# Kernel optimization log

Hardware: AMD Instinct MI355X
Metric: run time of the kernel (lower is better)

## Reference

```python
import jax, jax.numpy as jnp
import numpy as np

NUM_USERS = 100000
NUM_ITEMS = 50000
EMB_DIM = 64
NUM_LAYERS = 3
NUM_EDGES = 1000000


def _xavier(key, shape):
    fan_in, fan_out = shape[-1], shape[-2] if len(shape) > 1 else shape[-1]
    limit = float(np.sqrt(6.0 / (fan_in + fan_out)))
    return jax.random.uniform(key, shape, jnp.float32, -limit, limit)


def setup_inputs() -> dict:
    key = jax.random.key(0)
    ks = jax.random.split(key, 8)
    edge_u = jax.random.randint(ks[0], (NUM_EDGES,), 0, NUM_USERS)
    edge_i = jax.random.randint(ks[1], (NUM_EDGES,), 0, NUM_ITEMS)
    u_emb = _xavier(ks[2], (NUM_USERS, EMB_DIM))
    i_emb = _xavier(ks[3], (NUM_ITEMS, EMB_DIM))
    Wgc = _xavier(ks[4], (NUM_LAYERS, EMB_DIM, EMB_DIM))
    Wbi = _xavier(ks[5], (NUM_LAYERS, EMB_DIM, EMB_DIM))
    bgc = jnp.zeros((NUM_LAYERS, EMB_DIM), jnp.float32)
    bbi = jnp.zeros((NUM_LAYERS, EMB_DIM), jnp.float32)
    return {"u_emb": u_emb, "i_emb": i_emb, "Wgc": Wgc, "bgc": bgc,
            "Wbi": Wbi, "bbi": bbi, "edge_u": edge_u, "edge_i": edge_i}


def _smooth(X, src, dst, dv_isqrt, de_inv, num_v, num_e):
    # HGNN smoothing: D_v^{-1/2} H D_e^{-1} H^T D_v^{-1/2} X via edge list
    X1 = X * dv_isqrt[:, None]
    E = jax.ops.segment_sum(X1[src], dst, num_segments=num_e) * de_inv[:, None]
    Y = jax.ops.segment_sum(E[dst], src, num_segments=num_v)
    return Y * dv_isqrt[:, None]


def reference(u_emb, i_emb, Wgc, bgc, Wbi, bbi, edge_u, edge_i):
    NU, NI, D = u_emb.shape[0], i_emb.shape[0], u_emb.shape[1]
    ones = jnp.ones((edge_u.shape[0],), jnp.float32)
    deg_u = jax.ops.segment_sum(ones, edge_u, num_segments=NU)
    deg_i = jax.ops.segment_sum(ones, edge_i, num_segments=NI)
    du_isqrt = jnp.where(deg_u > 0, deg_u, 1.0) ** -0.5 * (deg_u > 0)
    di_isqrt = jnp.where(deg_i > 0, deg_i, 1.0) ** -0.5 * (deg_i > 0)
    du_inv = jnp.where(deg_u > 0, 1.0 / jnp.where(deg_u > 0, deg_u, 1.0), 0.0)
    di_inv = jnp.where(deg_i > 0, 1.0 / jnp.where(deg_i > 0, deg_i, 1.0), 0.0)

    all_embs = jnp.concatenate([u_emb, i_emb], axis=0)
    embs_list = [all_embs]
    for l in range(Wgc.shape[0]):
        u, i = all_embs[:NU], all_embs[NU:]
        # hg_ui: users = vertices, items = hyperedges
        u_s = _smooth(u, edge_u, edge_i, du_isqrt, di_inv, NU, NI)
        # hg_iu: items = vertices, users = hyperedges
        i_s = _smooth(i, edge_i, edge_u, di_isqrt, du_inv, NI, NU)
        g = jnp.concatenate([u_s, i_s], axis=0)
        sum_embs = jax.nn.leaky_relu(g @ Wgc[l].T + bgc[l] + all_embs, negative_slope=0.2)
        bi_embs = jax.nn.leaky_relu((all_embs * g) @ Wbi[l].T + bbi[l], negative_slope=0.2)
        all_embs = sum_embs + bi_embs  # dropout off (eval mode)
        norm = jnp.sqrt(jnp.sum(all_embs * all_embs, axis=1, keepdims=True))
        all_embs = all_embs / jnp.maximum(norm, 1e-12)
        embs_list.append(all_embs)
    embs = jnp.mean(jnp.stack(embs_list, axis=1), axis=1)
    return embs[:NU], embs[NU:]
```

## Files before the change

### kernel.cpp

```cpp
#include <hip/hip_runtime.h>
#include <cstdint>
#include <cstddef>

#define NU 100000
#define NI 50000
#define NTOT 150000
#define EDIM 64
#define NE 1000000
#define NLAYERS 3
#define NTILES (NTOT / 16)
#define NPAIR (NTOT / 2)

#define NBKT 256
#define NPB 586
#define NSHARD 1
#define BCAP 13312
#define BCUR_STRIDE 16
#define BIN_EPB 1024
#define BIN_NBLK ((NE + BIN_EPB - 1) / BIN_EPB)
#define LCAP 28
#define LPAD 29
#define SLICE_CAP 13312

typedef __attribute__((ext_vector_type(8))) short short8;
typedef __attribute__((ext_vector_type(4))) float floatx4;

__device__ inline unsigned short f2bf(float f) {
    unsigned u = __float_as_uint(f);
    u += 0x7fffu + ((u >> 16) & 1u);
    return (unsigned short)(u >> 16);
}
__device__ inline unsigned pack_bf2(float a, float b) {
    unsigned ua = __float_as_uint(a); ua += 0x7fffu + ((ua >> 16) & 1u);
    unsigned ub = __float_as_uint(b); ub += 0x7fffu + ((ub >> 16) & 1u);
    return (ua >> 16) | (ub & 0xffff0000u);
}
__device__ inline float bf_lo(unsigned u) { return __uint_as_float(u << 16); }
__device__ inline float bf_hi(unsigned u) { return __uint_as_float(u & 0xffff0000u); }

__global__ __launch_bounds__(256) void k_binpairs(const int* __restrict__ eu,
                                                  const int* __restrict__ ei,
                                                  unsigned* __restrict__ bcur,
                                                  unsigned* __restrict__ bbuf) {
    __shared__ unsigned lbuf[NBKT * LPAD];
    __shared__ int lcnt[NBKT];
    int t = threadIdx.x;
    if (t < NBKT) lcnt[t] = 0;
    __syncthreads();
    int ebase = blockIdx.x * BIN_EPB + t;
#pragma unroll
    for (int k = 0; k < 4; ++k) {
        int e = ebase + k * 256;
        if (e < NE) {
            int u = eu[e];
            int v = NU + ei[e];
            int b0 = u / NPB;
            int w0 = ((u - b0 * NPB) << 18) | v;
            int p0 = atomicAdd(&lcnt[b0], 1);
            if (p0 < LCAP) lbuf[b0 * LPAD + p0] = (unsigned)w0;
            else {
                unsigned gp = atomicAdd(&bcur[b0 * BCUR_STRIDE], 1u);
                if (gp < BCAP) bbuf[(size_t)b0 * BCAP + gp] = (unsigned)w0;
            }
            int b1 = v / NPB;
            int w1 = ((v - b1 * NPB) << 18) | u;
            int p1 = atomicAdd(&lcnt[b1], 1);
            if (p1 < LCAP) lbuf[b1 * LPAD + p1] = (unsigned)w1;
            else {
                unsigned gp = atomicAdd(&bcur[b1 * BCUR_STRIDE], 1u);
                if (gp < BCAP) bbuf[(size_t)b1 * BCAP + gp] = (unsigned)w1;
            }
        }
    }
    __syncthreads();
    int nb = min(lcnt[t], LCAP);
    if (nb > 0) {
        unsigned gp = atomicAdd(&bcur[t * BCUR_STRIDE], (unsigned)nb);
        for (int i = 0; i < nb; ++i) {
            unsigned idx = gp + i;
            if (idx < BCAP) bbuf[(size_t)t * BCAP + idx] = lbuf[t * LPAD + i];
        }
    }
}

__global__ void k_bktprefix(const unsigned* __restrict__ bcur, int* __restrict__ bktbase) {
    __shared__ int sm[256];
    int t = threadIdx.x;
    int tot = (int)bcur[t * BCUR_STRIDE];
    if (tot > BCAP) tot = BCAP;
    sm[t] = tot;
    __syncthreads();
    for (int off = 1; off < 256; off <<= 1) {
        int tmp = (t >= off) ? sm[t - off] : 0;
        __syncthreads();
        sm[t] += tmp;
        __syncthreads();
    }
    bktbase[t] = sm[t] - tot;
}

__global__ __launch_bounds__(1024) void k_buildcsr(
    const unsigned* __restrict__ bbuf, const unsigned* __restrict__ bcur,
    const int* __restrict__ bktbase, int* __restrict__ deg, int* __restrict__ start,
    float* __restrict__ isq, float* __restrict__ inv, int* __restrict__ csr) {
    __shared__ int slice[SLICE_CAP];
    __shared__ int lcur[NPB];
    __shared__ int scnt_s;
    int b = blockIdx.x;
    int t = threadIdx.x;
    int n0 = b * NPB;
    int nn = NTOT - n0;
    if (nn > NPB) nn = NPB;
    if (nn < 0) nn = 0;
    if (t < NPB) lcur[t] = 0;
    if (t == 0) {
        int c = (int)bcur[b * BCUR_STRIDE];
        scnt_s = c < BCAP ? c : BCAP;
    }
    __syncthreads();
    int c = scnt_s;
    const unsigned* pb = bbuf + (size_t)b * BCAP;
    for (int i = t; i < c; i += 1024) atomicAdd(&lcur[(int)(pb[i] >> 18)], 1);
    __syncthreads();
    int cnt_t = (t < nn) ? lcur[t] : 0;
    slice[t] = cnt_t;
    __syncthreads();
    for (int off = 1; off < 1024; off <<= 1) {
        int tmp = (t >= off) ? slice[t - off] : 0;
        __syncthreads();
        slice[t] += tmp;
        __syncthreads();
    }
    int excl = slice[t] - cnt_t;
    int slen = slice[1023];
    int bb = bktbase[b];
    if (t < nn) {
        int n = n0 + t;
        deg[n] = cnt_t;
        start[n] = bb + excl;
        float df = (float)cnt_t;
        isq[n] = cnt_t > 0 ? 1.0f / sqrtf(df) : 0.f;
        inv[n] = cnt_t > 0 ? 1.0f / df : 0.f;
    }
    __syncthreads();
    if (t < nn) lcur[t] = excl;
    __syncthreads();
    for (int i = t; i < c; i += 1024) {
        unsigned pr = pb[i];
        int idx = atomicAdd(&lcur[(int)(pr >> 18)], 1);
        if (idx < SLICE_CAP) slice[idx] = (int)(pr & 0x3FFFFu);
    }
    __syncthreads();
    if (slen > SLICE_CAP) slen = SLICE_CAP;
    for (int i = t; i < slen; i += 1024) csr[bb + i] = slice[i];
}

__global__ void k_init(const float* __restrict__ ue, const float* __restrict__ ie,
                       const float* __restrict__ isq,
                       unsigned* __restrict__ snap0, unsigned* gbuf,
                       const float* __restrict__ Wg, const float* __restrict__ Wb,
                       unsigned short* __restrict__ wgb, unsigned short* __restrict__ wbb,
                       unsigned* __restrict__ Ebuf) {
    int i = blockIdx.x * blockDim.x + threadIdx.x;
    const int n4 = NTOT * EDIM / 4;
    const int nw4 = NLAYERS * 4096 / 4;
    if (i < nw4) {
        float4 g4 = ((const float4*)Wg)[i];
        float4 b4 = ((const float4*)Wb)[i];
        uint2 g, b;
        g.x = pack_bf2(g4.x, g4.y); g.y = pack_bf2(g4.z, g4.w);
        b.x = pack_bf2(b4.x, b4.y); b.y = pack_bf2(b4.z, b4.w);
        ((uint2*)wgb)[i] = g;
        ((uint2*)wbb)[i] = b;
    }
    if (i < 16) {
        ((uint2*)(Ebuf + NTOT * 32))[i] = make_uint2(0u, 0u);
        ((uint2*)(gbuf + NTOT * 32))[i] = make_uint2(0u, 0u);
    }
    if (i < n4) {
        const int nu4 = NU * EDIM / 4;
        float4 v = (i < nu4) ? ((const float4*)ue)[i] : ((const float4*)ie)[i - nu4];
        float s = isq[i >> 4];
        uint2 b, bs;
        b.x = pack_bf2(v.x, v.y);
        b.y = pack_bf2(v.z, v.w);
        bs.x = pack_bf2(v.x * s, v.y * s);
        bs.y = pack_bf2(v.z * s, v.w * s);
        ((uint2*)snap0)[i] = b;
        ((uint2*)gbuf)[i] = bs;
    }
}

__global__ __launch_bounds__(256) void k_gather(
    const unsigned* __restrict__ in_bf, unsigned* __restrict__ out_bf,
    const int* __restrict__ csr, const int* __restrict__ start,
    const int* __restrict__ deg, const float* __restrict__ sA) {
    int gw = (blockIdx.x * 256 + threadIdx.x) >> 6;
    int lane = threadIdx.x & 63;
    if (gw >= NPAIR) return;
    int l2 = lane & 31;
    int hbase = lane & 32;
    int row = gw * 2 + (lane >> 5);
    int s0 = start[row];
    int dg = deg[row];
    int dgo = __shfl_xor(dg, 32);
    int dgmax = max(dg, dgo);
    float acc0 = 0.f, acc1 = 0.f;
    for (int j0 = 0; j0 < dgmax; j0 += 32) {
        int nidx = NTOT;
        if (j0 + l2 < dg) nidx = csr[s0 + j0 + l2];
        int jlim = min(32, dgmax - j0);
        for (int j = 0; j < jlim; j += 16) {
            int mm[16];
            unsigned uu[16];
#pragma unroll
            for (int k = 0; k < 16; ++k)
                mm[k] = __shfl(nidx, hbase + j + k);
#pragma unroll
            for (int k = 0; k < 16; ++k)
                uu[k] = in_bf[mm[k] * 32 + l2];
#pragma unroll
            for (int k = 0; k < 16; ++k) {
                acc0 += bf_lo(uu[k]);
                acc1 += bf_hi(uu[k]);
            }
        }
    }
    float s = sA[row];
    out_bf[row * 32 + l2] = pack_bf2(s * acc0, s * acc1);
}

__global__ __launch_bounds__(256) void k_dense_mfma(
    const unsigned short* __restrict__ a_prev, unsigned* gbuf,
    unsigned short* __restrict__ snap_l, const float* __restrict__ isq,
    const unsigned short* __restrict__ wgb, const unsigned short* __restrict__ wbb,
    const float* __restrict__ bg, const float* __restrict__ bb, int writeScaled,
    int finalOut, const unsigned short* __restrict__ s1,
    const float* __restrict__ ue, const float* __restrict__ ie,
    float* __restrict__ outp) {
    int lane = threadIdx.x & 63;
    int lanelo = lane & 15;
    int quad = lane >> 4;
    int wid = (blockIdx.x * blockDim.x + threadIdx.x) >> 6;
    if (wid >= NTILES) return;

    short8 bWg[4][2], bWb[4][2];
#pragma unroll
    for (int t = 0; t < 4; ++t) {
#pragma unroll
        for (int h = 0; h < 2; ++h) {
            int n = t * 16 + lanelo;
            int k0 = h * 32 + quad * 8;
            bWg[t][h] = *(const short8*)&wgb[n * 64 + k0];
            bWb[t][h] = *(const short8*)&wbb[n * 64 + k0];
        }
    }
    float bgv[4], bbv[4];
#pragma unroll
    for (int t = 0; t < 4; ++t) {
        bgv[t] = bg[t * 16 + lanelo];
        bbv[t] = bb[t * 16 + lanelo];
    }

    int rbase = wid * 16;
    int arow = rbase + lanelo;
    short8 aG[2], aAG[2];
#pragma unroll
    for (int h = 0; h < 2; ++h) {
        uint4 ug = *(const uint4*)(gbuf + arow * 32 + h * 16 + quad * 4);
        uint4 ua = *(const uint4*)((const unsigned*)a_prev + arow * 32 + h * 16 + quad * 4);
        aG[h] = *(const short8*)&ug;
        uint4 up;
        up.x = pack_bf2(bf_lo(ua.x) * bf_lo(ug.x), bf_hi(ua.x) * bf_hi(ug.x));
        up.y = pack_bf2(bf_lo(ua.y) * bf_lo(ug.y), bf_hi(ua.y) * bf_hi(ug.y));
        up.z = pack_bf2(bf_lo(ua.z) * bf_lo(ug.z), bf_hi(ua.z) * bf_hi(ug.z));
        up.w = pack_bf2(bf_lo(ua.w) * bf_lo(ug.w), bf_hi(ua.w) * bf_hi(ug.w));
        aAG[h] = *(const short8*)&up;
    }
    floatx4 accg[4], accb[4];
#pragma unroll
    for (int t = 0; t < 4; ++t) {
        accg[t] = (floatx4)(0.f);
        accb[t] = (floatx4)(0.f);
    }
#pragma unroll
    for (int t = 0; t < 4; ++t) {
#pragma unroll
        for (int h = 0; h < 2; ++h) {
            accg[t] = __builtin_amdgcn_mfma_f32_16x16x32_bf16(aG[h], bWg[t][h], accg[t], 0, 0, 0);
            accb[t] = __builtin_amdgcn_mfma_f32_16x16x32_bf16(aAG[h], bWb[t][h], accb[t], 0, 0, 0);
        }
    }
    float nv[4][4];
    float ss[4] = {0.f, 0.f, 0.f, 0.f};
#pragma unroll
    for (int i = 0; i < 4; ++i) {
        int r = rbase + quad * 4 + i;
#pragma unroll
        for (int t = 0; t < 4; ++t) {
            float a = __uint_as_float((unsigned)a_prev[r * 64 + t * 16 + lanelo] << 16);
            float e1 = accg[t][i] + bgv[t] + a;
            e1 = e1 >= 0.f ? e1 : 0.2f * e1;
            float e2 = accb[t][i] + bbv[t];
            e2 = e2 >= 0.f ? e2 : 0.2f * e2;
            float v = e1 + e2;
            nv[i][t] = v;
            ss[i] += v * v;
        }
    }
#pragma unroll
    for (int m = 1; m < 16; m <<= 1) {
#pragma unroll
        for (int i = 0; i < 4; ++i) ss[i] += __shfl_xor(ss[i], m, 64);
    }
#pragma unroll
    for (int i = 0; i < 4; ++i) {
        int r = rbase + quad * 4 + i;
        float rn = 1.0f / fmaxf(sqrtf(ss[i]), 1e-12f);
        float sc = isq[r] * rn;
        if (finalOut) {
#pragma unroll
            for (int t = 0; t < 4; ++t) {
                int idx = r * 64 + t * 16 + lanelo;
                float rr = nv[i][t] * rn;
                float s1v = __uint_as_float((unsigned)s1[idx] << 16);
                float s2v = __uint_as_float((unsigned)a_prev[idx] << 16);
                float ev = (r < NU) ? ue[idx] : ie[idx - NU * 64];
                outp[idx] = 0.25f * (ev + s1v + s2v + rr);
            }
        } else {
#pragma unroll
            for (int t = 0; t < 4; ++t) {
                int idx = r * 64 + t * 16 + lanelo;
                float rr = nv[i][t] * rn;
                snap_l[idx] = f2bf(rr);
                if (writeScaled)
                    ((unsigned short*)gbuf)[idx] = f2bf(nv[i][t] * sc);
            }
        }
    }
}


extern "C" void kernel_launch(void* const* d_in, const int* in_sizes, int n_in,
                              void* d_out, int out_size, void* d_ws, size_t ws_size,
                              hipStream_t stream) {
    const float* u_emb = (const float*)d_in[0];
    const float* i_emb = (const float*)d_in[1];
    const float* Wgc = (const float*)d_in[2];
    const float* bgc = (const float*)d_in[3];
    const float* Wbi = (const float*)d_in[4];
    const float* bbi = (const float*)d_in[5];
    const int* edge_u = (const int*)d_in[6];
    const int* edge_i = (const int*)d_in[7];
    float* out = (float*)d_out;

    char* w = (char*)d_ws;
    auto alloc = [&](size_t bytes) {
        char* p = w;
        w += (bytes + 255) & ~(size_t)255;
        return p;
    };
    const size_t ROWBYTES = (size_t)(NTOT + 1) * EDIM * 2;
    int* deg = (int*)alloc((size_t)NTOT * 4);
    int* start = (int*)alloc((size_t)NTOT * 4);
    unsigned* bcur = (unsigned*)alloc((size_t)NBKT * BCUR_STRIDE * 4);
    int* bktbase = (int*)alloc(256 * 4);
    int* csr = (int*)alloc((size_t)2 * NE * 4);
    float* isq = (float*)alloc((size_t)NTOT * 4);
    float* inv = (float*)alloc((size_t)NTOT * 4);
    unsigned short* wgb = (unsigned short*)alloc((size_t)NLAYERS * 4096 * 2);
    unsigned short* wbb = (unsigned short*)alloc((size_t)NLAYERS * 4096 * 2);
    unsigned* snap0 = (unsigned*)alloc((size_t)NTOT * EDIM * 2);
    unsigned* snap1 = (unsigned*)alloc((size_t)NTOT * EDIM * 2);
    unsigned* snap2 = (unsigned*)alloc((size_t)NTOT * EDIM * 2);
    unsigned* Ebuf = (unsigned*)alloc(ROWBYTES);
    unsigned* gbuf = (unsigned*)alloc(ROWBYTES);
    unsigned* bbuf = (unsigned*)snap1;

    hipMemsetAsync(bcur, 0, (size_t)NBKT * BCUR_STRIDE * 4, stream);
    k_binpairs<<<BIN_NBLK, 256, 0, stream>>>(edge_u, edge_i, bcur, bbuf);
    k_bktprefix<<<1, 256, 0, stream>>>(bcur, bktbase);
    k_buildcsr<<<NBKT, 1024, 0, stream>>>(bbuf, bcur, bktbase, deg, start, isq, inv, csr);
    k_init<<<(NTOT * EDIM / 4 + 255) / 256, 256, 0, stream>>>(
        u_emb, i_emb, isq, snap0, gbuf, Wgc, Wbi, wgb, wbb, Ebuf);

    const int gatherBlocks = (NPAIR * 64 + 255) / 256;
    const int denseBlocks = (NTILES * 64 + 255) / 256;
    const unsigned short* aprev[3] = {(unsigned short*)snap0, (unsigned short*)snap1,
                                      (unsigned short*)snap2};
    unsigned short* snaps[3] = {(unsigned short*)snap1, (unsigned short*)snap2,
                                (unsigned short*)snap1 };
    for (int l = 0; l < NLAYERS; ++l) {
        k_gather<<<gatherBlocks, 256, 0, stream>>>(gbuf, Ebuf, csr, start, deg, inv);
        k_gather<<<gatherBlocks, 256, 0, stream>>>(Ebuf, gbuf, csr, start, deg, isq);
        k_dense_mfma<<<denseBlocks, 256, 0, stream>>>(
            aprev[l], gbuf, snaps[l], isq, wgb + (size_t)l * 4096, wbb + (size_t)l * 4096,
            bgc + (size_t)l * 64, bbi + (size_t)l * 64,
            l < NLAYERS - 1 ? 1 : 0,
            l == NLAYERS - 1 ? 1 : 0,
            (const unsigned short*)snap1, u_emb, i_emb, out);
    }
}
```

Baseline: 468.4 us.

## Fuse second gather into dense MFMA kernel and fold prefix/init into CSR build

Removes the second per-layer gather kernel by having the dense MFMA kernel compute each row's neighbor sum from the CSR directly in its A-fragment layout, so the intermediate gbuf no longer makes a round trip through memory. Also folds the bucket prefix scan and the embedding/weight bf16 init into the CSR build kernel, cutting two launches. In exchange the gather inside the dense kernel uses 16 lanes per row with 4-deep unrolling, so it may expose less memory parallelism and suffer load imbalance from the max degree across 16 rows. Init work is now concentrated in 256 large blocks instead of many small ones.

```diff
diff --git a/kernel.cpp b/kernel.cpp
--- a/kernel.cpp
+++ b/kernel.cpp
@@ -13,7 +13,6 @@
 
 #define NBKT 256
 #define NPB 586
-#define NSHARD 1
 #define BCAP 13312
 #define BCUR_STRIDE 16
 #define BIN_EPB 1024
@@ -83,42 +82,42 @@
     }
 }
 
-__global__ void k_bktprefix(const unsigned* __restrict__ bcur, int* __restrict__ bktbase) {
-    __shared__ int sm[256];
-    int t = threadIdx.x;
-    int tot = (int)bcur[t * BCUR_STRIDE];
-    if (tot > BCAP) tot = BCAP;
-    sm[t] = tot;
-    __syncthreads();
-    for (int off = 1; off < 256; off <<= 1) {
-        int tmp = (t >= off) ? sm[t - off] : 0;
-        __syncthreads();
-        sm[t] += tmp;
-        __syncthreads();
-    }
-    bktbase[t] = sm[t] - tot;
-}
-
 __global__ __launch_bounds__(1024) void k_buildcsr(
     const unsigned* __restrict__ bbuf, const unsigned* __restrict__ bcur,
-    const int* __restrict__ bktbase, int* __restrict__ deg, int* __restrict__ start,
-    float* __restrict__ isq, float* __restrict__ inv, int* __restrict__ csr) {
+    int* __restrict__ deg, int* __restrict__ start,
+    float* __restrict__ isq, float* __restrict__ inv, int* __restrict__ csr,
+    const float* __restrict__ ue, const float* __restrict__ ie,
+    unsigned* __restrict__ snap0, unsigned* __restrict__ gbuf,
+    unsigned* __restrict__ Ebuf,
+    const float* __restrict__ Wg, const float* __restrict__ Wb,
+    unsigned short* __restrict__ wgb, unsigned short* __restrict__ wbb) {
     __shared__ int slice[SLICE_CAP];
     __shared__ int lcur[NPB];
-    __shared__ int scnt_s;
+    __shared__ float sisq[NPB];
+    __shared__ int bb_s, scnt_s;
     int b = blockIdx.x;
     int t = threadIdx.x;
     int n0 = b * NPB;
     int nn = NTOT - n0;
     if (nn > NPB) nn = NPB;
     if (nn < 0) nn = 0;
+    if (t < NBKT) slice[t] = min((int)bcur[t * BCUR_STRIDE], BCAP);
     if (t < NPB) lcur[t] = 0;
+    __syncthreads();
+    for (int off = 1; off < NBKT; off <<= 1) {
+        int tmp = (t < NBKT && t >= off) ? slice[t - off] : 0;
+        __syncthreads();
+        if (t < NBKT) slice[t] += tmp;
+        __syncthreads();
+    }
     if (t == 0) {
-        int c = (int)bcur[b * BCUR_STRIDE];
-        scnt_s = c < BCAP ? c : BCAP;
+        int tb = min((int)bcur[b * BCUR_STRIDE], BCAP);
+        scnt_s = tb;
+        bb_s = slice[b] - tb;
     }
     __syncthreads();
     int c = scnt_s;
+    int bb = bb_s;
     const unsigned* pb = bbuf + (size_t)b * BCAP;
     for (int i = t; i < c; i += 1024) atomicAdd(&lcur[(int)(pb[i] >> 18)], 1);
     __syncthreads();
@@ -133,13 +132,14 @@
     }
     int excl = slice[t] - cnt_t;
     int slen = slice[1023];
-    int bb = bktbase[b];
     if (t < nn) {
         int n = n0 + t;
         deg[n] = cnt_t;
         start[n] = bb + excl;
         float df = (float)cnt_t;
-        isq[n] = cnt_t > 0 ? 1.0f / sqrtf(df) : 0.f;
+        float q = cnt_t > 0 ? 1.0f / sqrtf(df) : 0.f;
+        isq[n] = q;
+        sisq[t] = q;
         inv[n] = cnt_t > 0 ? 1.0f / df : 0.f;
     }
     __syncthreads();
@@ -153,41 +153,34 @@
     __syncthreads();
     if (slen > SLICE_CAP) slen = SLICE_CAP;
     for (int i = t; i < slen; i += 1024) csr[bb + i] = slice[i];
-}
-
-__global__ void k_init(const float* __restrict__ ue, const float* __restrict__ ie,
-                       const float* __restrict__ isq,
-                       unsigned* __restrict__ snap0, unsigned* gbuf,
-                       const float* __restrict__ Wg, const float* __restrict__ Wb,
-                       unsigned short* __restrict__ wgb, unsigned short* __restrict__ wbb,
-                       unsigned* __restrict__ Ebuf) {
-    int i = blockIdx.x * blockDim.x + threadIdx.x;
-    const int n4 = NTOT * EDIM / 4;
-    const int nw4 = NLAYERS * 4096 / 4;
-    if (i < nw4) {
-        float4 g4 = ((const float4*)Wg)[i];
-        float4 b4 = ((const float4*)Wb)[i];
-        uint2 g, b;
-        g.x = pack_bf2(g4.x, g4.y); g.y = pack_bf2(g4.z, g4.w);
-        b.x = pack_bf2(b4.x, b4.y); b.y = pack_bf2(b4.z, b4.w);
-        ((uint2*)wgb)[i] = g;
-        ((uint2*)wbb)[i] = b;
-    }
-    if (i < 16) {
-        ((uint2*)(Ebuf + NTOT * 32))[i] = make_uint2(0u, 0u);
-        ((uint2*)(gbuf + NTOT * 32))[i] = make_uint2(0u, 0u);
-    }
-    if (i < n4) {
-        const int nu4 = NU * EDIM / 4;
-        float4 v = (i < nu4) ? ((const float4*)ue)[i] : ((const float4*)ie)[i - nu4];
-        float s = isq[i >> 4];
-        uint2 b, bs;
-        b.x = pack_bf2(v.x, v.y);
-        b.y = pack_bf2(v.z, v.w);
+    for (int idx = t; idx < nn * 16; idx += 1024) {
+        int r = idx >> 4, cc = idx & 15;
+        int n = n0 + r;
+        float4 v = (n < NU) ? ((const float4*)ue)[(size_t)n * 16 + cc]
+                            : ((const float4*)ie)[(size_t)(n - NU) * 16 + cc];
+        float s = sisq[r];
+        uint2 bq, bs;
+        bq.x = pack_bf2(v.x, v.y);
+        bq.y = pack_bf2(v.z, v.w);
         bs.x = pack_bf2(v.x * s, v.y * s);
         bs.y = pack_bf2(v.z * s, v.w * s);
-        ((uint2*)snap0)[i] = b;
-        ((uint2*)gbuf)[i] = bs;
+        ((uint2*)snap0)[(size_t)n * 16 + cc] = bq;
+        ((uint2*)gbuf)[(size_t)n * 16 + cc] = bs;
+    }
+    if (b == 0) {
+        for (int i = t; i < NLAYERS * 4096 / 4; i += 1024) {
+            float4 g4 = ((const float4*)Wg)[i];
+            float4 b4 = ((const float4*)Wb)[i];
+            uint2 g, bq;
+            g.x = pack_bf2(g4.x, g4.y); g.y = pack_bf2(g4.z, g4.w);
+            bq.x = pack_bf2(b4.x, b4.y); bq.y = pack_bf2(b4.z, b4.w);
+            ((uint2*)wgb)[i] = g;
+            ((uint2*)wbb)[i] = bq;
+        }
+        if (t < 16) {
+            ((uint2*)(Ebuf + NTOT * 32))[t] = make_uint2(0u, 0u);
+            ((uint2*)(gbuf + NTOT * 32))[t] = make_uint2(0u, 0u);
+        }
     }
 }
 
@@ -230,9 +223,12 @@
     out_bf[row * 32 + l2] = pack_bf2(s * acc0, s * acc1);
 }
 
-__global__ __launch_bounds__(256) void k_dense_mfma(
+__global__ __launch_bounds__(256) void k_dense_fused(
+    const unsigned* __restrict__ Ebuf,
     const unsigned short* __restrict__ a_prev, unsigned* gbuf,
     unsigned short* __restrict__ snap_l, const float* __restrict__ isq,
+    const int* __restrict__ csr, const int* __restrict__ start,
+    const int* __restrict__ deg,
     const unsigned short* __restrict__ wgb, const unsigned short* __restrict__ wbb,
     const float* __restrict__ bg, const float* __restrict__ bb, int writeScaled,
     int finalOut, const unsigned short* __restrict__ s1,
@@ -243,6 +239,50 @@
     int quad = lane >> 4;
     int wid = (blockIdx.x * blockDim.x + threadIdx.x) >> 6;
     if (wid >= NTILES) return;
+    int rbase = wid * 16;
+    int arow = rbase + lanelo;
+
+    int s0 = start[arow];
+    int dg = deg[arow];
+    int dmax = dg;
+#pragma unroll
+    for (int m = 1; m < 16; m <<= 1) dmax = max(dmax, __shfl_xor(dmax, m));
+    float accL[2][4], accH[2][4];
+#pragma unroll
+    for (int h = 0; h < 2; ++h)
+#pragma unroll
+        for (int j = 0; j < 4; ++j) { accL[h][j] = 0.f; accH[h][j] = 0.f; }
+    for (int i = 0; i < dmax; i += 4) {
+        int mm[4];
+#pragma unroll
+        for (int k = 0; k < 4; ++k)
+            mm[k] = (i + k < dg) ? csr[s0 + i + k] : NTOT;
+        uint4 ea[4], eb[4];
+#pragma unroll
+        for (int k = 0; k < 4; ++k) {
+            ea[k] = *(const uint4*)(Ebuf + (size_t)mm[k] * 32 + quad * 4);
+            eb[k] = *(const uint4*)(Ebuf + (size_t)mm[k] * 32 + 16 + quad * 4);
+        }
+#pragma unroll
+        for (int k = 0; k < 4; ++k) {
+            const unsigned* pa = (const unsigned*)&ea[k];
+            const unsigned* pcb = (const unsigned*)&eb[k];
+#pragma unroll
+            for (int j = 0; j < 4; ++j) {
+                accL[0][j] += bf_lo(pa[j]);  accH[0][j] += bf_hi(pa[j]);
+                accL[1][j] += bf_lo(pcb[j]); accH[1][j] += bf_hi(pcb[j]);
+            }
+        }
+    }
+    float sc0 = isq[arow];
+    uint4 ugq[2];
+#pragma unroll
+    for (int h = 0; h < 2; ++h) {
+        unsigned* w4 = (unsigned*)&ugq[h];
+#pragma unroll
+        for (int j = 0; j < 4; ++j)
+            w4[j] = pack_bf2(sc0 * accL[h][j], sc0 * accH[h][j]);
+    }
 
     short8 bWg[4][2], bWb[4][2];
 #pragma unroll
@@ -261,13 +301,10 @@
         bgv[t] = bg[t * 16 + lanelo];
         bbv[t] = bb[t * 16 + lanelo];
     }
-
-    int rbase = wid * 16;
-    int arow = rbase + lanelo;
     short8 aG[2], aAG[2];
 #pragma unroll
     for (int h = 0; h < 2; ++h) {
-        uint4 ug = *(const uint4*)(gbuf + arow * 32 + h * 16 + quad * 4);
+        uint4 ug = ugq[h];
         uint4 ua = *(const uint4*)((const unsigned*)a_prev + arow * 32 + h * 16 + quad * 4);
         aG[h] = *(const short8*)&ug;
         uint4 up;
@@ -365,7 +402,6 @@
     int* deg = (int*)alloc((size_t)NTOT * 4);
     int* start = (int*)alloc((size_t)NTOT * 4);
     unsigned* bcur = (unsigned*)alloc((size_t)NBKT * BCUR_STRIDE * 4);
-    int* bktbase = (int*)alloc(256 * 4);
     int* csr = (int*)alloc((size_t)2 * NE * 4);
     float* isq = (float*)alloc((size_t)NTOT * 4);
     float* inv = (float*)alloc((size_t)NTOT * 4);
@@ -380,10 +416,9 @@
 
     hipMemsetAsync(bcur, 0, (size_t)NBKT * BCUR_STRIDE * 4, stream);
     k_binpairs<<<BIN_NBLK, 256, 0, stream>>>(edge_u, edge_i, bcur, bbuf);
-    k_bktprefix<<<1, 256, 0, stream>>>(bcur, bktbase);
-    k_buildcsr<<<NBKT, 1024, 0, stream>>>(bbuf, bcur, bktbase, deg, start, isq, inv, csr);
-    k_init<<<(NTOT * EDIM / 4 + 255) / 256, 256, 0, stream>>>(
-        u_emb, i_emb, isq, snap0, gbuf, Wgc, Wbi, wgb, wbb, Ebuf);
+    k_buildcsr<<<NBKT, 1024, 0, stream>>>(bbuf, bcur, deg, start, isq, inv, csr,
+                                          u_emb, i_emb, snap0, gbuf, Ebuf,
+                                          Wgc, Wbi, wgb, wbb);
 
     const int gatherBlocks = (NPAIR * 64 + 255) / 256;
     const int denseBlocks = (NTILES * 64 + 255) / 256;
@@ -393,9 +428,9 @@
                                 (unsigned short*)snap1 };
     for (int l = 0; l < NLAYERS; ++l) {
         k_gather<<<gatherBlocks, 256, 0, stream>>>(gbuf, Ebuf, csr, start, deg, inv);
-        k_gather<<<gatherBlocks, 256, 0, stream>>>(Ebuf, gbuf, csr, start, deg, isq);
-        k_dense_mfma<<<denseBlocks, 256, 0, stream>>>(
-            aprev[l], gbuf, snaps[l], isq, wgb + (size_t)l * 4096, wbb + (size_t)l * 4096,
+        k_dense_fused<<<denseBlocks, 256, 0, stream>>>(
+            Ebuf, aprev[l], gbuf, snaps[l], isq, csr, start, deg,
+            wgb + (size_t)l * 4096, wbb + (size_t)l * 4096,
             bgc + (size_t)l * 64, bbi + (size_t)l * 64,
             l < NLAYERS - 1 ? 1 : 0,
             l == NLAYERS - 1 ? 1 : 0,
```

After: 503.7 us. +7.5%, slower.
